# Kernel optimization log

Hardware: AMD Instinct MI355X
Metric: run time of the kernel (lower is better)

## Reference

```python
import jax, jax.numpy as jnp
import numpy as np

H = 8        # num_heads
D = 64       # qkv_dim
E = 512      # embed_dim = H*D
MS = 16      # ms_hidden_dim


def setup_inputs() -> dict:
    key = jax.random.key(0)
    ks = jax.random.split(key, 12)
    b, r, c = 4, 512, 512
    row_emb = jax.random.normal(ks[0], (b, r, E), dtype=jnp.float32)
    col_emb = jax.random.normal(ks[1], (b, c, E), dtype=jnp.float32)
    cost_mat = jax.random.uniform(ks[2], (b, r, c), dtype=jnp.float32)
    attn_mask = jax.random.randint(ks[3], (b, H, r, c), 0, 2) > 0
    s = 1.0 / np.sqrt(E)
    Wq = jax.random.uniform(ks[4], (H * D, E), minval=-s, maxval=s)
    Wk = jax.random.uniform(ks[5], (H * D, E), minval=-s, maxval=s)
    Wv = jax.random.uniform(ks[6], (H * D, E), minval=-s, maxval=s)
    Wout = jax.random.uniform(ks[7], (E, E), minval=-s, maxval=s)
    m1 = np.sqrt(0.5)
    m2 = np.sqrt(1.0 / MS)
    Wmix1 = jax.random.uniform(ks[8], (H * MS, 2 * H), minval=-m1, maxval=m1)
    Wmix2 = jax.random.uniform(ks[9], (H, H * MS), minval=-m2, maxval=m2)
    return {"row_emb": row_emb, "col_emb": col_emb, "cost_mat": cost_mat,
            "attn_mask": attn_mask, "Wq": Wq, "Wk": Wk, "Wv": Wv,
            "Wmix1": Wmix1, "Wmix2": Wmix2, "Wout": Wout}


def reference(row_emb, col_emb, cost_mat, attn_mask, Wq, Wk, Wv, Wmix1, Wmix2, Wout):
    b, r, _ = row_emb.shape
    c = col_emb.shape[1]
    norm = 1.0 / jnp.sqrt(jnp.asarray(D, row_emb.dtype))
    # projections -> [b, h, s, d]
    q = (row_emb @ Wq.T).reshape(b, r, H, D).transpose(0, 2, 1, 3)
    k = (col_emb @ Wk.T).reshape(b, c, H, D).transpose(0, 2, 1, 3)
    v = (col_emb @ Wv.T).reshape(b, c, H, D).transpose(0, 2, 1, 3)
    dot = norm * jnp.einsum('bhrd,bhcd->bhrc', q, k)            # [b,h,r,c]
    cost = jnp.broadcast_to(cost_mat[:, None, :, :], dot.shape)  # [b,h,r,c]
    # stack then rearrange 'b h r c s -> b r c (h s)' (h major, s minor)
    two = jnp.stack([dot, cost], axis=-1)                        # [b,h,r,c,2]
    two = two.transpose(0, 2, 3, 1, 4).reshape(b, r, c, 2 * H)
    hid = jax.nn.relu(two @ Wmix1.T)                             # [b,r,c,H*MS]
    ms = hid @ Wmix2.T                                           # [b,r,c,H]
    logits = ms.transpose(0, 3, 1, 2)                            # [b,h,r,c]
    # mask handling: rows that are fully masked become fully unmasked
    all_masked = jnp.all(attn_mask, axis=-1, keepdims=True)
    mask = jnp.where(all_masked, False, attn_mask)
    logits = jnp.where(mask, -jnp.inf, logits)
    weights = jax.nn.softmax(logits, axis=-1)
    out = jnp.einsum('bhrc,bhcd->bhrd', weights, v)              # [b,h,r,d]
    out = out.transpose(0, 2, 1, 3).reshape(b, r, H * D)         # b s (h d)
    return out @ Wout.T
```

## Files before the change

kernel.cpp:

```cpp
#include <hip/hip_runtime.h>
#include <math.h>

typedef __attribute__((ext_vector_type(8))) short bf16x8;
typedef __attribute__((ext_vector_type(4))) float f32x4;
typedef unsigned short ushort_t;

static __device__ inline unsigned short f2bf(float f) {
    union { float f; unsigned u; } v; v.f = f;
    unsigned r = v.u + 0x7fff + ((v.u >> 16) & 1);
    return (unsigned short)(r >> 16);
}

#if defined(__has_builtin)
#  if __has_builtin(__builtin_amdgcn_cvt_pk_bf16_f32)
#    define HAVE_PK_BF16 1
#  endif
#endif

static __device__ inline unsigned pk2bf(float a, float b) {
#ifdef HAVE_PK_BF16
    auto r = __builtin_amdgcn_cvt_pk_bf16_f32(a, b);
    unsigned u; __builtin_memcpy(&u, &r, 4);
    return u;
#else
    return (unsigned)f2bf(a) | ((unsigned)f2bf(b) << 16);
#endif
}

__global__ __launch_bounds__(256) void convert_all(const float* __restrict__ a0,
                                                   const float* __restrict__ a1,
                                                   const float* __restrict__ a2,
                                                   const float* __restrict__ a3,
                                                   const float* __restrict__ a4,
                                                   const float* __restrict__ a5,
                                                   ushort_t* __restrict__ dst) {
    const size_t e = ((size_t)blockIdx.x * 256 + threadIdx.x) * 4;
    const float* src; size_t off;
    if      (e < 1048576) { src = a0; off = 0; }
    else if (e < 2097152) { src = a1; off = 1048576; }
    else if (e < 2359296) { src = a2; off = 2097152; }
    else if (e < 2621440) { src = a3; off = 2359296; }
    else if (e < 2883584) { src = a4; off = 2621440; }
    else                  { src = a5; off = 2883584; }
    const float4 v = *(const float4*)(src + (e - off));
    uint2 o; o.x = pk2bf(v.x, v.y); o.y = pk2bf(v.z, v.w);
    *(uint2*)(dst + e) = o;
}

__global__ __launch_bounds__(256) void gemm_qkv(const ushort_t* __restrict__ rowb,
                                                const ushort_t* __restrict__ colb,
                                                const ushort_t* __restrict__ Wqb,
                                                const ushort_t* __restrict__ Wkb,
                                                const ushort_t* __restrict__ Wvb,
                                                ushort_t* __restrict__ Qb,
                                                ushort_t* __restrict__ Kb,
                                                ushort_t* __restrict__ Vt) {
    const int z = blockIdx.z;
    const ushort_t* A = (z == 0) ? rowb : colb;
    const ushort_t* B = (z == 0) ? Wqb : (z == 1) ? Wkb : Wvb;

    const int t    = threadIdx.x;
    const int w    = t >> 6;
    const int lane = t & 63;
    const int quad = lane >> 4;
    const int sl   = lane & 15;
    const int m0 = blockIdx.x * 64 + (w >> 1) * 32;
    const int n0 = blockIdx.y * 64 + (w & 1) * 32;

    f32x4 acc[2][2] = {};

    for (int k0 = 0; k0 < 512; k0 += 32) {
        bf16x8 a[2], b[2];
#pragma unroll
        for (int rs = 0; rs < 2; ++rs)
            a[rs] = *(const bf16x8*)(A + (size_t)(m0 + rs * 16 + sl) * 512 + k0 + quad * 8);
#pragma unroll
        for (int cs = 0; cs < 2; ++cs)
            b[cs] = *(const bf16x8*)(B + (size_t)(n0 + cs * 16 + sl) * 512 + k0 + quad * 8);
#pragma unroll
        for (int rs = 0; rs < 2; ++rs)
#pragma unroll
            for (int cs = 0; cs < 2; ++cs)
                acc[rs][cs] = __builtin_amdgcn_mfma_f32_16x16x32_bf16(a[rs], b[cs], acc[rs][cs], 0, 0, 0);
    }

#pragma unroll
    for (int rs = 0; rs < 2; ++rs)
#pragma unroll
        for (int cs = 0; cs < 2; ++cs) {
            const int n = n0 + cs * 16 + sl;
            if (z == 2) {
                const int mb   = m0 + rs * 16 + quad * 4;
                const int bidx = mb >> 9, c = mb & 511;
                const int h = n >> 6, d = n & 63;
                ushort4 o;
                o.x = f2bf(acc[rs][cs][0]); o.y = f2bf(acc[rs][cs][1]);
                o.z = f2bf(acc[rs][cs][2]); o.w = f2bf(acc[rs][cs][3]);
                *(ushort4*)(Vt + (size_t)(((bidx * 8 + h) * 64 + d)) * 512 + c) = o;
            } else {
                ushort_t* C = (z == 0) ? Qb : Kb;
#pragma unroll
                for (int reg = 0; reg < 4; ++reg) {
                    const int m = m0 + rs * 16 + quad * 4 + reg;
                    C[(size_t)m * 512 + n] = f2bf(acc[rs][cs][reg]);
                }
            }
        }
}

__global__ __launch_bounds__(256) void gemm_out(const ushort_t* __restrict__ A,
                                                const ushort_t* __restrict__ B,
                                                float* __restrict__ C) {
    const int t    = threadIdx.x;
    const int w    = t >> 6;
    const int lane = t & 63;
    const int quad = lane >> 4;
    const int sl   = lane & 15;
    const int m0 = blockIdx.x * 64 + (w >> 1) * 32;
    const int n0 = blockIdx.y * 64 + (w & 1) * 32;

    f32x4 acc[2][2] = {};

    for (int k0 = 0; k0 < 512; k0 += 32) {
        bf16x8 a[2], b[2];
#pragma unroll
        for (int rs = 0; rs < 2; ++rs)
            a[rs] = *(const bf16x8*)(A + (size_t)(m0 + rs * 16 + sl) * 512 + k0 + quad * 8);
#pragma unroll
        for (int cs = 0; cs < 2; ++cs)
            b[cs] = *(const bf16x8*)(B + (size_t)(n0 + cs * 16 + sl) * 512 + k0 + quad * 8);
#pragma unroll
        for (int rs = 0; rs < 2; ++rs)
#pragma unroll
            for (int cs = 0; cs < 2; ++cs)
                acc[rs][cs] = __builtin_amdgcn_mfma_f32_16x16x32_bf16(a[rs], b[cs], acc[rs][cs], 0, 0, 0);
    }

#pragma unroll
    for (int rs = 0; rs < 2; ++rs)
#pragma unroll
        for (int cs = 0; cs < 2; ++cs) {
            const int n = n0 + cs * 16 + sl;
#pragma unroll
            for (int reg = 0; reg < 4; ++reg) {
                const int m = m0 + rs * 16 + quad * 4 + reg;
                C[(size_t)m * 512 + n] = acc[rs][cs][reg];
            }
        }
}

__global__ __launch_bounds__(512) void dot_mlp_v5(const ushort_t* __restrict__ Qb,
                                                  const ushort_t* __restrict__ Kb,
                                                  const float* __restrict__ cost,
                                                  const float* __restrict__ W1,
                                                  const float* __restrict__ W2,
                                                  float* __restrict__ logits) {
    __shared__ ushort_t Xs[1024 * 18];
    __shared__ ushort_t W1fs[128 * 16];
    __shared__ ushort_t W2ss[8 * 128];

    const int b  = blockIdx.z;
    const int r0 = blockIdx.y * 32;
    const int c0 = blockIdx.x * 32;
    const int t    = threadIdx.x;
    const int w    = t >> 6;
    const int lane = t & 63;
    const int quad = lane >> 4;
    const int sl   = lane & 15;

    const bf16x8 zf = {0, 0, 0, 0, 0, 0, 0, 0};

    if (t < 128) {
        float s = 0.f;
#pragma unroll
        for (int h = 0; h < 8; ++h) {
            W1fs[t * 16 + h] = f2bf(W1[t * 16 + 2 * h]);
            s += W1[t * 16 + 2 * h + 1];
        }
        W1fs[t * 16 + 8] = f2bf(s);
#pragma unroll
        for (int k = 9; k < 16; ++k) W1fs[t * 16 + k] = 0;
    }
#pragma unroll
    for (int i = 0; i < 2; ++i) W2ss[t + i * 512] = f2bf(W2[t + i * 512]);

#pragma unroll
    for (int i = 0; i < 2; ++i) {
        const int cell = t + i * 512;
        const int rl = cell >> 5, cl = cell & 31;
        unsigned* base = (unsigned*)(Xs + cell * 18 + 8);
        base[0] = (unsigned)f2bf(cost[((size_t)b * 512 + r0 + rl) * 512 + c0 + cl]);
        base[1] = 0; base[2] = 0; base[3] = 0; base[4] = 0;
    }

    {
        const int h = w;
        bf16x8 af[2][2], bfr[2][2];
#pragma unroll
        for (int rs = 0; rs < 2; ++rs)
#pragma unroll
            for (int ks = 0; ks < 2; ++ks)
                af[rs][ks] = *(const bf16x8*)(Qb +
                    ((size_t)(b * 512 + r0 + rs * 16 + sl) * 512 + h * 64 + ks * 32 + quad * 8));
#pragma unroll
        for (int cs = 0; cs < 2; ++cs)
#pragma unroll
            for (int ks = 0; ks < 2; ++ks)
                bfr[cs][ks] = *(const bf16x8*)(Kb +
                    ((size_t)(b * 512 + c0 + cs * 16 + sl) * 512 + h * 64 + ks * 32 + quad * 8));
#pragma unroll
        for (int rs = 0; rs < 2; ++rs)
#pragma unroll
            for (int cs = 0; cs < 2; ++cs) {
                f32x4 acc = {0.f, 0.f, 0.f, 0.f};
                acc = __builtin_amdgcn_mfma_f32_16x16x32_bf16(af[rs][0], bfr[cs][0], acc, 0, 0, 0);
                acc = __builtin_amdgcn_mfma_f32_16x16x32_bf16(af[rs][1], bfr[cs][1], acc, 0, 0, 0);
#pragma unroll
                for (int reg = 0; reg < 4; ++reg) {
                    const int cell = (rs * 16 + quad * 4 + reg) * 32 + cs * 16 + sl;
                    Xs[cell * 18 + h] = f2bf(acc[reg] * 0.125f);
                }
            }
    }

    __syncthreads();

    bf16x8 aw1[8];
#pragma unroll
    for (int nt = 0; nt < 8; ++nt)
        aw1[nt] = (quad < 2) ? *(const bf16x8*)&W1fs[(nt * 16 + sl) * 16 + quad * 8] : zf;

    bf16x8 w2f[4];
#pragma unroll
    for (int ks = 0; ks < 4; ++ks) {
        union { ushort_t s[8]; bf16x8 v; } tu;
#pragma unroll
        for (int i = 0; i < 8; ++i) {
            const int j = (2 * ks + (i >> 2)) * 16 + quad * 4 + (i & 3);
            tu.s[i] = (sl < 8) ? W2ss[sl * 128 + j] : (ushort_t)0;
        }
        w2f[ks] = tu.v;
    }

#pragma unroll
    for (int mt = 0; mt < 8; ++mt) {
        const int gmt = w * 8 + mt;
        const int cb  = gmt * 16;

        bf16x8 a1 = zf;
        if (quad < 2) {
            const unsigned* xr = (const unsigned*)Xs + (size_t)(cb + sl) * 9 + quad * 4;
            union { unsigned u[4]; bf16x8 v; } tmp;
            tmp.u[0] = xr[0]; tmp.u[1] = xr[1]; tmp.u[2] = xr[2]; tmp.u[3] = xr[3];
            a1 = tmp.v;
        }

        f32x4 hT[8];
#pragma unroll
        for (int j = 0; j < 8; ++j) {
            f32x4 z = {0.f, 0.f, 0.f, 0.f};
            hT[j] = __builtin_amdgcn_mfma_f32_16x16x32_bf16(aw1[j], a1, z, 0, 0, 0);
        }

        f32x4 acc2 = {0.f, 0.f, 0.f, 0.f};
#pragma unroll
        for (int ks = 0; ks < 4; ++ks) {
            union { unsigned u[4]; bf16x8 v; } hb;
            hb.u[0] = pk2bf(fmaxf(hT[2 * ks][0], 0.f),     fmaxf(hT[2 * ks][1], 0.f));
            hb.u[1] = pk2bf(fmaxf(hT[2 * ks][2], 0.f),     fmaxf(hT[2 * ks][3], 0.f));
            hb.u[2] = pk2bf(fmaxf(hT[2 * ks + 1][0], 0.f), fmaxf(hT[2 * ks + 1][1], 0.f));
            hb.u[3] = pk2bf(fmaxf(hT[2 * ks + 1][2], 0.f), fmaxf(hT[2 * ks + 1][3], 0.f));
            acc2 = __builtin_amdgcn_mfma_f32_16x16x32_bf16(w2f[ks], hb.v, acc2, 0, 0, 0);
        }

        if (quad < 2) {
            const int r = r0 + (gmt >> 1);
            const int c = c0 + (gmt & 1) * 16 + sl;
#pragma unroll
            for (int reg = 0; reg < 4; ++reg) {
                const int h = quad * 4 + reg;
                logits[((size_t)(b * 8 + h) * 512 + r) * 512 + c] = acc2[reg];
            }
        }
    }
}

__global__ __launch_bounds__(256) void softmax_pv(const float* __restrict__ logits,
                                                  const int* __restrict__ mask,
                                                  const ushort_t* __restrict__ Vt,
                                                  ushort_t* __restrict__ Aout) {
    __shared__ ushort_t Ps[32 * 520];

    const int t    = threadIdx.x;
    const int w    = t >> 6;
    const int lane = t & 63;
    const int quad = lane >> 4;
    const int sl   = lane & 15;
    const int rt = blockIdx.x;
    const int bh = blockIdx.y;
    const int r0 = rt * 32;

#pragma unroll
    for (int rr = 0; rr < 8; ++rr) {
        const int row = w * 8 + rr;
        const float* lp = logits + ((size_t)bh * 512 + r0 + row) * 512;
        const int*   mp = mask   + ((size_t)bh * 512 + r0 + row) * 512;

        float v[8]; int m[8]; int allm = 1;
#pragma unroll
        for (int i = 0; i < 8; ++i) {
            v[i] = lp[lane + i * 64];
            m[i] = mp[lane + i * 64];
            allm &= (m[i] != 0);
        }
        const bool all_masked = (__all(allm) != 0);

        float mx = -__builtin_inff();
#pragma unroll
        for (int i = 0; i < 8; ++i) {
            const bool keep = all_masked || (m[i] == 0);
            if (keep) mx = fmaxf(mx, v[i]);
        }
#pragma unroll
        for (int s = 32; s > 0; s >>= 1) mx = fmaxf(mx, __shfl_xor(mx, s, 64));

        float e[8]; float sum = 0.f;
#pragma unroll
        for (int i = 0; i < 8; ++i) {
            const bool keep = all_masked || (m[i] == 0);
            e[i] = keep ? __expf(v[i] - mx) : 0.f;
            sum += e[i];
        }
#pragma unroll
        for (int s = 32; s > 0; s >>= 1) sum += __shfl_xor(sum, s, 64);

        const float inv = 1.f / sum;
#pragma unroll
        for (int i = 0; i < 8; ++i)
            Ps[row * 520 + lane + i * 64] = f2bf(e[i] * inv);
    }

    __syncthreads();

    const int mt  = w >> 1;
    const int n0w = (w & 1) * 32;
    const ushort_t* vb = Vt + (size_t)bh * 64 * 512;

    f32x4 acc[2] = {};
    for (int ks = 0; ks < 16; ++ks) {
        union { uint2 u2[2]; bf16x8 v; } ta;
        const ushort_t* pp = Ps + (size_t)(mt * 16 + sl) * 520 + ks * 32 + quad * 8;
        ta.u2[0] = *(const uint2*)pp;
        ta.u2[1] = *(const uint2*)(pp + 4);
        bf16x8 bv[2];
#pragma unroll
        for (int cn = 0; cn < 2; ++cn)
            bv[cn] = *(const bf16x8*)(vb + (size_t)(n0w + cn * 16 + sl) * 512 + ks * 32 + quad * 8);
#pragma unroll
        for (int cn = 0; cn < 2; ++cn)
            acc[cn] = __builtin_amdgcn_mfma_f32_16x16x32_bf16(ta.v, bv[cn], acc[cn], 0, 0, 0);
    }

    const int bidx = bh >> 3, h = bh & 7;
    ushort_t* Cb = Aout + (size_t)bidx * 512 * 512 + h * 64;
#pragma unroll
    for (int cn = 0; cn < 2; ++cn) {
        const int n = n0w + cn * 16 + sl;
#pragma unroll
        for (int reg = 0; reg < 4; ++reg) {
            const int m = r0 + mt * 16 + quad * 4 + reg;
            Cb[(size_t)m * 512 + n] = f2bf(acc[cn][reg]);
        }
    }
}

extern "C" void kernel_launch(void* const* d_in, const int* in_sizes, int n_in,
                              void* d_out, int out_size, void* d_ws, size_t ws_size,
                              hipStream_t stream) {
    const float* row_emb = (const float*)d_in[0];
    const float* col_emb = (const float*)d_in[1];
    const float* cost    = (const float*)d_in[2];
    const int*   mask    = (const int*)d_in[3];
    const float* Wq      = (const float*)d_in[4];
    const float* Wk      = (const float*)d_in[5];
    const float* Wv      = (const float*)d_in[6];
    const float* Wmix1   = (const float*)d_in[7];
    const float* Wmix2   = (const float*)d_in[8];
    const float* Wout    = (const float*)d_in[9];
    float* out = (float*)d_out;

    char* ws = (char*)d_ws;
    const size_t MB = (size_t)1 << 20;
    ushort_t* convDst = (ushort_t*)ws;
    ushort_t* rowb  = (ushort_t*)(ws);
    ushort_t* colb  = (ushort_t*)(ws + 2 * MB);
    ushort_t* Wqb   = (ushort_t*)(ws + 4 * MB);
    ushort_t* Wkb   = (ushort_t*)(ws + 4 * MB + 512 * 1024);
    ushort_t* Wvb   = (ushort_t*)(ws + 5 * MB);
    ushort_t* Woutb = (ushort_t*)(ws + 5 * MB + 512 * 1024);
    ushort_t* Qb    = (ushort_t*)(ws + 6 * MB);
    ushort_t* Kb    = (ushort_t*)(ws + 8 * MB);
    ushort_t* Vt    = (ushort_t*)(ws + 10 * MB);
    ushort_t* Aoutb = (ushort_t*)(ws + 12 * MB);
    float* logitsBuf = (float*)(ws + 40 * MB);

    convert_all<<<3072, 256, 0, stream>>>(row_emb, col_emb, Wq, Wk, Wv, Wout, convDst);

    gemm_qkv<<<dim3(32, 8, 3), 256, 0, stream>>>(rowb, colb, Wqb, Wkb, Wvb, Qb, Kb, Vt);

    dot_mlp_v5<<<dim3(16, 16, 4), 512, 0, stream>>>(Qb, Kb, cost, Wmix1, Wmix2, logitsBuf);

    softmax_pv<<<dim3(16, 32), 256, 0, stream>>>(logitsBuf, mask, Vt, Aoutb);

    gemm_out<<<dim3(32, 8), 256, 0, stream>>>(Aoutb, Woutb, out);
}
```

Before: 183.7 us.

## Retile dot-MLP to 32x16 blocks and vectorize softmax loads and LDS stores

The dot+MLP kernel is retiled to 32x16 cells per block with 256 threads, doubling the grid. Each wave now computes two heads per pass and writes packed bf16 pairs into a 20-short-stride LDS layout. The MLP loop interleaves the first-layer MFMAs with the ReLU/pack and second-layer MFMA, which lowers peak register use. The softmax kernel switches to float4/int4 loads for logits and mask, stores packed bf16 pairs into a re-padded LDS buffer, and partially unrolls the PV loop. The trade-off is redundant W1/W2 staging across twice as many blocks and a changed lane-to-column mapping in softmax.

```diff
diff --git a/kernel.cpp b/kernel.cpp
--- a/kernel.cpp
+++ b/kernel.cpp
@@ -149,19 +149,19 @@
         }
 }
 
-__global__ __launch_bounds__(512) void dot_mlp_v5(const ushort_t* __restrict__ Qb,
+__global__ __launch_bounds__(256) void dot_mlp_v6(const ushort_t* __restrict__ Qb,
                                                   const ushort_t* __restrict__ Kb,
                                                   const float* __restrict__ cost,
                                                   const float* __restrict__ W1,
                                                   const float* __restrict__ W2,
                                                   float* __restrict__ logits) {
-    __shared__ ushort_t Xs[1024 * 18];
+    __shared__ ushort_t Xs[512 * 20];
     __shared__ ushort_t W1fs[128 * 16];
     __shared__ ushort_t W2ss[8 * 128];
 
     const int b  = blockIdx.z;
     const int r0 = blockIdx.y * 32;
-    const int c0 = blockIdx.x * 32;
+    const int c0 = blockIdx.x * 16;
     const int t    = threadIdx.x;
     const int w    = t >> 6;
     const int lane = t & 63;
@@ -182,45 +182,51 @@
         for (int k = 9; k < 16; ++k) W1fs[t * 16 + k] = 0;
     }
 #pragma unroll
-    for (int i = 0; i < 2; ++i) W2ss[t + i * 512] = f2bf(W2[t + i * 512]);
+    for (int i = 0; i < 4; ++i) W2ss[t + i * 256] = f2bf(W2[t + i * 256]);
 
 #pragma unroll
     for (int i = 0; i < 2; ++i) {
-        const int cell = t + i * 512;
-        const int rl = cell >> 5, cl = cell & 31;
-        unsigned* base = (unsigned*)(Xs + cell * 18 + 8);
+        const int cell = t + i * 256;
+        const int rl = cell >> 4, cl = cell & 15;
+        unsigned* base = (unsigned*)(Xs + cell * 20) + 4;
         base[0] = (unsigned)f2bf(cost[((size_t)b * 512 + r0 + rl) * 512 + c0 + cl]);
-        base[1] = 0; base[2] = 0; base[3] = 0; base[4] = 0;
+        base[1] = 0; base[2] = 0; base[3] = 0;
     }
 
     {
-        const int h = w;
-        bf16x8 af[2][2], bfr[2][2];
-#pragma unroll
-        for (int rs = 0; rs < 2; ++rs)
-#pragma unroll
-            for (int ks = 0; ks < 2; ++ks)
-                af[rs][ks] = *(const bf16x8*)(Qb +
-                    ((size_t)(b * 512 + r0 + rs * 16 + sl) * 512 + h * 64 + ks * 32 + quad * 8));
-#pragma unroll
-        for (int cs = 0; cs < 2; ++cs)
-#pragma unroll
-            for (int ks = 0; ks < 2; ++ks)
-                bfr[cs][ks] = *(const bf16x8*)(Kb +
-                    ((size_t)(b * 512 + c0 + cs * 16 + sl) * 512 + h * 64 + ks * 32 + quad * 8));
-#pragma unroll
-        for (int rs = 0; rs < 2; ++rs)
-#pragma unroll
-            for (int cs = 0; cs < 2; ++cs) {
-                f32x4 acc = {0.f, 0.f, 0.f, 0.f};
-                acc = __builtin_amdgcn_mfma_f32_16x16x32_bf16(af[rs][0], bfr[cs][0], acc, 0, 0, 0);
-                acc = __builtin_amdgcn_mfma_f32_16x16x32_bf16(af[rs][1], bfr[cs][1], acc, 0, 0, 0);
-#pragma unroll
-                for (int reg = 0; reg < 4; ++reg) {
-                    const int cell = (rs * 16 + quad * 4 + reg) * 32 + cs * 16 + sl;
-                    Xs[cell * 18 + h] = f2bf(acc[reg] * 0.125f);
+        const int rs  = w >> 1;
+        const int hbj = w & 1;
+        unsigned uu[2][4];
+#pragma unroll
+        for (int hp = 0; hp < 2; ++hp) {
+            const int h0 = hbj * 4 + hp * 2;
+            bf16x8 qa[2][2], ka[2][2];
+#pragma unroll
+            for (int hh = 0; hh < 2; ++hh)
+#pragma unroll
+                for (int ks = 0; ks < 2; ++ks) {
+                    qa[hh][ks] = *(const bf16x8*)(Qb +
+                        ((size_t)(b * 512 + r0 + rs * 16 + sl) * 512 + (h0 + hh) * 64 + ks * 32 + quad * 8));
+                    ka[hh][ks] = *(const bf16x8*)(Kb +
+                        ((size_t)(b * 512 + c0 + sl) * 512 + (h0 + hh) * 64 + ks * 32 + quad * 8));
                 }
-            }
+            f32x4 ac0 = {0.f, 0.f, 0.f, 0.f}, ac1 = {0.f, 0.f, 0.f, 0.f};
+            ac0 = __builtin_amdgcn_mfma_f32_16x16x32_bf16(qa[0][0], ka[0][0], ac0, 0, 0, 0);
+            ac0 = __builtin_amdgcn_mfma_f32_16x16x32_bf16(qa[0][1], ka[0][1], ac0, 0, 0, 0);
+            ac1 = __builtin_amdgcn_mfma_f32_16x16x32_bf16(qa[1][0], ka[1][0], ac1, 0, 0, 0);
+            ac1 = __builtin_amdgcn_mfma_f32_16x16x32_bf16(qa[1][1], ka[1][1], ac1, 0, 0, 0);
+#pragma unroll
+            for (int reg = 0; reg < 4; ++reg)
+                uu[hp][reg] = pk2bf(ac0[reg] * 0.125f, ac1[reg] * 0.125f);
+        }
+        const int rowb = rs * 16 + quad * 4;
+#pragma unroll
+        for (int reg = 0; reg < 4; ++reg) {
+            const int cell = (rowb + reg) * 16 + sl;
+            unsigned* xp = (unsigned*)(Xs + cell * 20) + hbj * 2;
+            xp[0] = uu[0][reg];
+            xp[1] = uu[1][reg];
+        }
     }
 
     __syncthreads();
@@ -244,38 +250,34 @@
 
 #pragma unroll
     for (int mt = 0; mt < 8; ++mt) {
-        const int gmt = w * 8 + mt;
-        const int cb  = gmt * 16;
+        const int gmt  = w * 8 + mt;
+        const int cell = gmt * 16 + sl;
 
         bf16x8 a1 = zf;
         if (quad < 2) {
-            const unsigned* xr = (const unsigned*)Xs + (size_t)(cb + sl) * 9 + quad * 4;
+            const unsigned* xr = (const unsigned*)Xs + (size_t)cell * 10 + quad * 4;
             union { unsigned u[4]; bf16x8 v; } tmp;
             tmp.u[0] = xr[0]; tmp.u[1] = xr[1]; tmp.u[2] = xr[2]; tmp.u[3] = xr[3];
             a1 = tmp.v;
         }
 
-        f32x4 hT[8];
-#pragma unroll
-        for (int j = 0; j < 8; ++j) {
+        f32x4 acc2 = {0.f, 0.f, 0.f, 0.f};
+#pragma unroll
+        for (int ks = 0; ks < 4; ++ks) {
             f32x4 z = {0.f, 0.f, 0.f, 0.f};
-            hT[j] = __builtin_amdgcn_mfma_f32_16x16x32_bf16(aw1[j], a1, z, 0, 0, 0);
-        }
-
-        f32x4 acc2 = {0.f, 0.f, 0.f, 0.f};
-#pragma unroll
-        for (int ks = 0; ks < 4; ++ks) {
+            const f32x4 h0v = __builtin_amdgcn_mfma_f32_16x16x32_bf16(aw1[2 * ks],     a1, z, 0, 0, 0);
+            const f32x4 h1v = __builtin_amdgcn_mfma_f32_16x16x32_bf16(aw1[2 * ks + 1], a1, z, 0, 0, 0);
             union { unsigned u[4]; bf16x8 v; } hb;
-            hb.u[0] = pk2bf(fmaxf(hT[2 * ks][0], 0.f),     fmaxf(hT[2 * ks][1], 0.f));
-            hb.u[1] = pk2bf(fmaxf(hT[2 * ks][2], 0.f),     fmaxf(hT[2 * ks][3], 0.f));
-            hb.u[2] = pk2bf(fmaxf(hT[2 * ks + 1][0], 0.f), fmaxf(hT[2 * ks + 1][1], 0.f));
-            hb.u[3] = pk2bf(fmaxf(hT[2 * ks + 1][2], 0.f), fmaxf(hT[2 * ks + 1][3], 0.f));
+            hb.u[0] = pk2bf(fmaxf(h0v[0], 0.f), fmaxf(h0v[1], 0.f));
+            hb.u[1] = pk2bf(fmaxf(h0v[2], 0.f), fmaxf(h0v[3], 0.f));
+            hb.u[2] = pk2bf(fmaxf(h1v[0], 0.f), fmaxf(h1v[1], 0.f));
+            hb.u[3] = pk2bf(fmaxf(h1v[2], 0.f), fmaxf(h1v[3], 0.f));
             acc2 = __builtin_amdgcn_mfma_f32_16x16x32_bf16(w2f[ks], hb.v, acc2, 0, 0, 0);
         }
 
         if (quad < 2) {
-            const int r = r0 + (gmt >> 1);
-            const int c = c0 + (gmt & 1) * 16 + sl;
+            const int r = r0 + gmt;
+            const int c = c0 + sl;
 #pragma unroll
             for (int reg = 0; reg < 4; ++reg) {
                 const int h = quad * 4 + reg;
@@ -289,7 +291,7 @@
                                                   const int* __restrict__ mask,
                                                   const ushort_t* __restrict__ Vt,
                                                   ushort_t* __restrict__ Aout) {
-    __shared__ ushort_t Ps[32 * 520];
+    __shared__ ushort_t Ps[32 * 522];
 
     const int t    = threadIdx.x;
     const int w    = t >> 6;
@@ -306,13 +308,20 @@
         const float* lp = logits + ((size_t)bh * 512 + r0 + row) * 512;
         const int*   mp = mask   + ((size_t)bh * 512 + r0 + row) * 512;
 
-        float v[8]; int m[8]; int allm = 1;
-#pragma unroll
-        for (int i = 0; i < 8; ++i) {
-            v[i] = lp[lane + i * 64];
-            m[i] = mp[lane + i * 64];
-            allm &= (m[i] != 0);
-        }
+        const float4 f0 = ((const float4*)lp)[lane];
+        const float4 f1 = ((const float4*)lp)[lane + 64];
+        const int4   m0 = ((const int4*)mp)[lane];
+        const int4   m1 = ((const int4*)mp)[lane + 64];
+
+        float v[8]; int m[8];
+        v[0] = f0.x; v[1] = f0.y; v[2] = f0.z; v[3] = f0.w;
+        v[4] = f1.x; v[5] = f1.y; v[6] = f1.z; v[7] = f1.w;
+        m[0] = m0.x; m[1] = m0.y; m[2] = m0.z; m[3] = m0.w;
+        m[4] = m1.x; m[5] = m1.y; m[6] = m1.z; m[7] = m1.w;
+
+        int allm = 1;
+#pragma unroll
+        for (int i = 0; i < 8; ++i) allm &= (m[i] != 0);
         const bool all_masked = (__all(allm) != 0);
 
         float mx = -__builtin_inff();
@@ -335,9 +344,11 @@
         for (int s = 32; s > 0; s >>= 1) sum += __shfl_xor(sum, s, 64);
 
         const float inv = 1.f / sum;
-#pragma unroll
-        for (int i = 0; i < 8; ++i)
-            Ps[row * 520 + lane + i * 64] = f2bf(e[i] * inv);
+        unsigned* pr = (unsigned*)Ps + 261 * row + 2 * lane;
+        pr[0]   = pk2bf(e[0] * inv, e[1] * inv);
+        pr[1]   = pk2bf(e[2] * inv, e[3] * inv);
+        pr[128] = pk2bf(e[4] * inv, e[5] * inv);
+        pr[129] = pk2bf(e[6] * inv, e[7] * inv);
     }
 
     __syncthreads();
@@ -347,11 +358,14 @@
     const ushort_t* vb = Vt + (size_t)bh * 64 * 512;
 
     f32x4 acc[2] = {};
+#pragma unroll 4
     for (int ks = 0; ks < 16; ++ks) {
-        union { uint2 u2[2]; bf16x8 v; } ta;
-        const ushort_t* pp = Ps + (size_t)(mt * 16 + sl) * 520 + ks * 32 + quad * 8;
-        ta.u2[0] = *(const uint2*)pp;
-        ta.u2[1] = *(const uint2*)(pp + 4);
+        union { unsigned u[4]; bf16x8 v; } ta;
+        const ushort_t* pp = Ps + (size_t)(mt * 16 + sl) * 522 + ks * 32 + quad * 8;
+        ta.u[0] = *(const unsigned*)(pp);
+        ta.u[1] = *(const unsigned*)(pp + 2);
+        ta.u[2] = *(const unsigned*)(pp + 4);
+        ta.u[3] = *(const unsigned*)(pp + 6);
         bf16x8 bv[2];
 #pragma unroll
         for (int cn = 0; cn < 2; ++cn)
@@ -408,7 +422,7 @@
 
     gemm_qkv<<<dim3(32, 8, 3), 256, 0, stream>>>(rowb, colb, Wqb, Wkb, Wvb, Qb, Kb, Vt);
 
-    dot_mlp_v5<<<dim3(16, 16, 4), 512, 0, stream>>>(Qb, Kb, cost, Wmix1, Wmix2, logitsBuf);
+    dot_mlp_v6<<<dim3(32, 16, 4), 256, 0, stream>>>(Qb, Kb, cost, Wmix1, Wmix2, logitsBuf);
 
     softmax_pv<<<dim3(16, 32), 256, 0, stream>>>(logitsBuf, mask, Vt, Aoutb);
 
```

After: 184.8 us. About the same (+0.6%).
